# Kernel tuning notes

Hardware: AMD Instinct MI355X
Metric: run time of the kernel (lower is better)

Reference implementation:

```python
import jax, jax.numpy as jnp
import numpy as np

BATCH, SEQ, D_IN, D_OUT = 32, 1024, 128, 128
NEG_SLOPE = 0.1


def setup_inputs() -> dict:
    key = jax.random.key(0)
    k1, k2, k3, k4 = jax.random.split(key, 4)
    nodes = jax.random.normal(k1, (BATCH, SEQ, D_IN), dtype=jnp.float32)
    adjacent = jax.random.randint(k2, (BATCH, SEQ, SEQ), 0, 2, dtype=jnp.int32)
    W = jax.random.normal(k3, (D_IN, D_OUT), dtype=jnp.float32) / np.sqrt(D_IN)
    B = jax.random.normal(k4, (D_IN, D_OUT), dtype=jnp.float32) / np.sqrt(D_IN)
    return {"nodes": nodes, "adjacent": adjacent, "W": W, "B": B}


def reference(nodes, adjacent, W, B):
    # mask[b, out, in] = 1 if edge (out -> in) present
    mask = (adjacent != 0).astype(nodes.dtype)
    # counts[b, in] = in-degree (number of 'out' neighbors pooled per target node)
    counts = mask.sum(axis=1)                               # [b, s_in]
    # segment-sum of neighbor features: pooled[b, in, d] = sum_out mask * nodes[b, out, d]
    pooled = jnp.einsum('boi,bod->bid', mask, nodes)        # [b, s_in, d]
    # mean over neighbors; nodes with zero degree get no pooled contribution
    pooled = jnp.where(counts[..., None] > 0,
                       pooled / jnp.maximum(counts, 1.0)[..., None],
                       jnp.zeros((), dtype=nodes.dtype))
    updated = nodes @ B + pooled @ W                        # [b, s, d_out]
    return jax.nn.leaky_relu(updated, negative_slope=NEG_SLOPE)
```

## Files before the change

### kernel.cpp

```cpp
#include <hip/hip_runtime.h>
#include <hip/hip_bf16.h>

#define SEQ 1024
#define DIM 128
#define NEG_SLOPE 0.1f

typedef __bf16 bf16x8 __attribute__((ext_vector_type(8)));
typedef float f32x4v __attribute__((ext_vector_type(4)));

#define NT_ELEMS (32u * 128u * 1024u)

__device__ __forceinline__ unsigned short bfb(float f) {
    __bf16 h = (__bf16)f;
    return __builtin_bit_cast(unsigned short, h);
}
__device__ __forceinline__ unsigned mpack(int x0, int x1) {
    unsigned m0 = (x0 != 0) ? 0x3F80u : 0u;
    unsigned m1 = (x1 != 0) ? 0x3F80u : 0u;
    return m0 | (m1 << 16);
}

__global__ __launch_bounds__(256)
void transpose_nodes(const float* __restrict__ nodes, unsigned short* __restrict__ nt)
{
    __shared__ float lds[64][33];
    const int bid = blockIdx.x;
    const int b   = bid >> 6;
    const int ot  = (bid >> 2) & 15;
    const int dt  = bid & 3;
    const int o0  = ot * 64, d0 = dt * 32;
    const int tid = threadIdx.x;

    const float* src = nodes + ((size_t)b * SEQ + o0) * DIM + d0;
    #pragma unroll
    for (int p = 0; p < 8; ++p) {
        const int o = (tid >> 5) + p * 8;
        const int d = tid & 31;
        lds[o][d] = src[(size_t)o * DIM + d];
    }
    __syncthreads();
    unsigned short* dst = nt + ((size_t)b * DIM + d0) * SEQ + o0;
    #pragma unroll
    for (int p = 0; p < 4; ++p) {
        const int d  = (tid >> 5) + p * 8;
        const int o2 = (tid & 31) * 2;
        ushort2 v;
        v.x = bfb(lds[o2][d]);
        v.y = bfb(lds[o2 + 1][d]);
        *(ushort2*)(dst + (size_t)d * SEQ + o2) = v;
    }
}

__global__ __launch_bounds__(256)
void transpose_wb(const float* __restrict__ W, const float* __restrict__ Bm,
                  unsigned short* __restrict__ wt, unsigned short* __restrict__ bt)
{
    const int which = blockIdx.x & 1;
    const int slice = blockIdx.x >> 1;
    const float* in  = which ? Bm : W;
    unsigned short* out = which ? bt : wt;
    const int base = slice * 1024;
    #pragma unroll
    for (int r = 0; r < 4; ++r) {
        const int idx = base + r * 256 + threadIdx.x;
        const int d = idx >> 7, k = idx & 127;
        out[idx] = bfb(in[k * DIM + d]);
    }
}

union LdsU {
    unsigned short mask_t[2][64][72];
    unsigned short pooled[64][136];
};

__global__ __launch_bounds__(256, 2)
void gcn_fused(const float* __restrict__ nodes,
               const int* __restrict__ adj,
               const unsigned short* __restrict__ nt,
               const unsigned short* __restrict__ wt,
               const unsigned short* __restrict__ bt,
               float* __restrict__ out)
{
    __shared__ LdsU u;

    const int bid   = blockIdx.x;
    const int xcd   = bid & 7;
    const int slot  = bid >> 3;
    const int batch = ((slot >> 4) << 3) | xcd;
    const int mtile = slot & 15;
    const int i0    = mtile << 6;

    const int tid  = threadIdx.x;
    const int wave = tid >> 6;
    const int lane = tid & 63;
    const int wm   = wave >> 1;
    const int wn   = wave & 1;
    const int lrow = lane & 15;
    const int quad = lane >> 4;

    const int*   __restrict__ adj_b   = adj   + (size_t)batch * SEQ * SEQ;
    const float* __restrict__ nodes_b = nodes + (size_t)batch * SEQ * DIM;
    const unsigned short* __restrict__ nt_b = nt + (size_t)batch * DIM * SEQ;

    const int a_row = (tid >> 4) * 4;
    const int a_col = (tid & 15) * 4;

    f32x4v acc[2][4] = {};
    f32x4v acc_cnt[2] = {};

    bf16x8 ones;
    #pragma unroll
    for (int j = 0; j < 8; ++j) ones[j] = __builtin_bit_cast(__bf16, (unsigned short)0x3F80);

    int4 A[4];
    auto load_adj = [&](int o0) {
        const int* pa = adj_b + (size_t)(o0 + a_row) * SEQ + (i0 + a_col);
        #pragma unroll
        for (int r = 0; r < 4; ++r) A[r] = *(const int4*)(pa + (size_t)r * SEQ);
    };

    const int d_b0 = wn * 64 + lrow;

    load_adj(0);

    for (int n = 0; n < 16; ++n) {
        const int buf = n & 1;
        #pragma unroll
        for (int j = 0; j < 4; ++j) {
            uint2 w;
            w.x = mpack(((const int*)&A[0])[j], ((const int*)&A[1])[j]);
            w.y = mpack(((const int*)&A[2])[j], ((const int*)&A[3])[j]);
            *(uint2*)&u.mask_t[buf][a_col + j][a_row] = w;
        }
        if (n < 15) load_adj((n + 1) * 64);
        __syncthreads();

        const int o_base = n * 64;
        #pragma unroll
        for (int kk = 0; kk < 2; ++kk) {
            const int ko = kk * 32 + quad * 8;
            bf16x8 av[2], bv[4];
            av[0] = *(const bf16x8*)&u.mask_t[buf][wm * 32 + lrow][ko];
            av[1] = *(const bf16x8*)&u.mask_t[buf][wm * 32 + 16 + lrow][ko];
            #pragma unroll
            for (int nf = 0; nf < 4; ++nf)
                bv[nf] = *(const bf16x8*)(nt_b + (size_t)(d_b0 + nf * 16) * SEQ + o_base + ko);
            #pragma unroll
            for (int mf = 0; mf < 2; ++mf) {
                #pragma unroll
                for (int nf = 0; nf < 4; ++nf)
                    acc[mf][nf] = __builtin_amdgcn_mfma_f32_16x16x32_bf16(av[mf], bv[nf], acc[mf][nf], 0, 0, 0);
                acc_cnt[mf] = __builtin_amdgcn_mfma_f32_16x16x32_bf16(av[mf], ones, acc_cnt[mf], 0, 0, 0);
            }
        }
    }

    __syncthreads();
    #pragma unroll
    for (int mf = 0; mf < 2; ++mf) {
        #pragma unroll
        for (int r = 0; r < 4; ++r) {
            const int row = wm * 32 + mf * 16 + quad * 4 + r;
            const float cnt = acc_cnt[mf][r];
            const float inv = (cnt > 0.5f) ? 1.0f / cnt : 0.0f;
            #pragma unroll
            for (int nf = 0; nf < 4; ++nf) {
                const int col = wn * 64 + nf * 16 + lrow;
                u.pooled[row][col] = bfb(acc[mf][nf][r] * inv);
            }
        }
    }
    __syncthreads();

    f32x4v acc2[2][4] = {};

    #pragma unroll
    for (int ks = 0; ks < 4; ++ks) {
        const int k0 = ks * 32 + quad * 8;
        bf16x8 av[2], av2[2], bw[4], bb[4];
        #pragma unroll
        for (int mf = 0; mf < 2; ++mf) {
            av[mf] = *(const bf16x8*)&u.pooled[wm * 32 + mf * 16 + lrow][k0];
            const float* p = nodes_b + (size_t)(i0 + wm * 32 + mf * 16 + lrow) * DIM + k0;
            const float4 f1 = *(const float4*)p;
            const float4 f2 = *(const float4*)(p + 4);
            av2[mf][0] = (__bf16)f1.x; av2[mf][1] = (__bf16)f1.y;
            av2[mf][2] = (__bf16)f1.z; av2[mf][3] = (__bf16)f1.w;
            av2[mf][4] = (__bf16)f2.x; av2[mf][5] = (__bf16)f2.y;
            av2[mf][6] = (__bf16)f2.z; av2[mf][7] = (__bf16)f2.w;
        }
        #pragma unroll
        for (int nf = 0; nf < 4; ++nf) {
            bw[nf] = *(const bf16x8*)(wt + (size_t)(d_b0 + nf * 16) * DIM + k0);
            bb[nf] = *(const bf16x8*)(bt + (size_t)(d_b0 + nf * 16) * DIM + k0);
        }
        #pragma unroll
        for (int mf = 0; mf < 2; ++mf)
            #pragma unroll
            for (int nf = 0; nf < 4; ++nf) {
                acc2[mf][nf] = __builtin_amdgcn_mfma_f32_16x16x32_bf16(av[mf],  bw[nf], acc2[mf][nf], 0, 0, 0);
                acc2[mf][nf] = __builtin_amdgcn_mfma_f32_16x16x32_bf16(av2[mf], bb[nf], acc2[mf][nf], 0, 0, 0);
            }
    }

    float* out_b = out + (size_t)batch * SEQ * DIM;
    #pragma unroll
    for (int mf = 0; mf < 2; ++mf) {
        #pragma unroll
        for (int nf = 0; nf < 4; ++nf) {
            const int col = wn * 64 + nf * 16 + lrow;
            #pragma unroll
            for (int r = 0; r < 4; ++r) {
                const int row = i0 + wm * 32 + mf * 16 + quad * 4 + r;
                const float x = acc2[mf][nf][r];
                out_b[(size_t)row * DIM + col] = (x > 0.0f) ? x : NEG_SLOPE * x;
            }
        }
    }
}

extern "C" void kernel_launch(void* const* d_in, const int* in_sizes, int n_in,
                              void* d_out, int out_size, void* d_ws, size_t ws_size,
                              hipStream_t stream) {
    const float* nodes = (const float*)d_in[0];
    const int*   adj   = (const int*)d_in[1];
    const float* W     = (const float*)d_in[2];
    const float* Bm    = (const float*)d_in[3];
    float*       out   = (float*)d_out;

    unsigned short* nt = (unsigned short*)d_ws;
    unsigned short* wt = nt + NT_ELEMS;
    unsigned short* bt = wt + 16384;

    transpose_nodes<<<dim3(2048), dim3(256), 0, stream>>>(nodes, nt);
    transpose_wb<<<dim3(32), dim3(256), 0, stream>>>(W, Bm, wt, bt);
    gcn_fused<<<dim3(512), dim3(256), 0, stream>>>(nodes, adj, nt, wt, bt, out);
}
```

Baseline: 234.5 us.

## Quantize mask and nodes to FP8, pre-transpose adjacency, use FP8 MFMA

Adds a separate kernel that converts the int32 adjacency into a transposed FP8 (e4m3 one-value) byte mask, and stores transposed nodes as FP8 instead of bf16. The main kernel then reads both directly from global memory, with no LDS staging or barriers in the aggregation loop, and uses fp8 MFMA instructions. The intent is to cut bytes moved and LDS traffic in the hot loop. The cost is an extra full pass over the 128MB adjacency plus a 32MB write, and a much coarser FP8 quantization of node features that may hurt accuracy.

```diff
diff --git a/kernel.cpp b/kernel.cpp
--- a/kernel.cpp
+++ b/kernel.cpp
@@ -7,48 +7,105 @@
 
 typedef __bf16 bf16x8 __attribute__((ext_vector_type(8)));
 typedef float f32x4v __attribute__((ext_vector_type(4)));
-
-#define NT_ELEMS (32u * 128u * 1024u)
+typedef unsigned char uchar;
+
+#define MASKQ_BYTES ((size_t)32 * 1024 * 1024)
+#define NTQ_BYTES   ((size_t)32 * 128 * 1024)
 
 __device__ __forceinline__ unsigned short bfb(float f) {
     __bf16 h = (__bf16)f;
     return __builtin_bit_cast(unsigned short, h);
 }
-__device__ __forceinline__ unsigned mpack(int x0, int x1) {
-    unsigned m0 = (x0 != 0) ? 0x3F80u : 0u;
-    unsigned m1 = (x1 != 0) ? 0x3F80u : 0u;
-    return m0 | (m1 << 16);
+
+
+__device__ __forceinline__ uchar f32_to_e4m3(float f) {
+#if __has_builtin(__builtin_amdgcn_cvt_pk_fp8_f32)
+    int r = __builtin_amdgcn_cvt_pk_fp8_f32(f, f, 0, false);
+    return (uchar)(r & 0xff);
+#else
+    unsigned u = __builtin_bit_cast(unsigned, f);
+    unsigned s = (u >> 24) & 0x80;
+    int e = (u >> 23) & 0xff;
+    unsigned m = u & 0x7fffff;
+    int te = e - 120;
+    if (te >= 1) {
+        unsigned keep = m >> 20, rest = m & 0xfffff;
+        keep += (rest > 0x80000u) || (rest == 0x80000u && (keep & 1));
+        if (keep == 8) { keep = 0; ++te; }
+        if (te > 15) return (uchar)(s | 0x7e);
+        return (uchar)(s | (te << 3) | keep);
+    }
+    float af = f < 0 ? -f : f;
+    int q = (int)(af * 512.0f + 0.5f);
+    if (q > 7) q = 7;
+    return (uchar)(s | q);
+#endif
 }
 
 __global__ __launch_bounds__(256)
-void transpose_nodes(const float* __restrict__ nodes, unsigned short* __restrict__ nt)
+void transpose_adj(const int* __restrict__ adj, uchar* __restrict__ mq)
+{
+    __shared__ uchar lds[64][72];
+    const int b  = blockIdx.x >> 8;
+    const int ot = (blockIdx.x >> 4) & 15;
+    const int it = blockIdx.x & 15;
+    const int o0 = ot << 6, i0 = it << 6;
+    const int t  = threadIdx.x;
+
+    const int r0 = (t >> 4) << 2;
+    const int c0 = (t & 15) << 2;
+    const int* pa = adj + ((size_t)(b * SEQ + o0 + r0)) * SEQ + i0 + c0;
+    int4 A[4];
+    #pragma unroll
+    for (int r = 0; r < 4; ++r) A[r] = *(const int4*)(pa + (size_t)r * SEQ);
+
+    #pragma unroll
+    for (int c = 0; c < 4; ++c) {
+        unsigned w = 0;
+        w |= (((const int*)&A[0])[c] != 0 ? 0x38u : 0u);
+        w |= (((const int*)&A[1])[c] != 0 ? 0x38u : 0u) << 8;
+        w |= (((const int*)&A[2])[c] != 0 ? 0x38u : 0u) << 16;
+        w |= (((const int*)&A[3])[c] != 0 ? 0x38u : 0u) << 24;
+        *(unsigned*)&lds[c0 + c][r0] = w;
+    }
+    __syncthreads();
+
+    const int i_loc = t >> 2;
+    const int quad  = t & 3;
+    const uint2 lo = *(const uint2*)&lds[i_loc][quad * 8];
+    const uint2 hi = *(const uint2*)&lds[i_loc][32 + quad * 8];
+    uint4 outv; outv.x = lo.x; outv.y = lo.y; outv.z = hi.x; outv.w = hi.y;
+    *(uint4*)(mq + ((size_t)(b * SEQ + i0 + i_loc)) * SEQ + o0 + quad * 16) = outv;
+}
+
+__global__ __launch_bounds__(256)
+void transpose_nodes(const float* __restrict__ nodes, uchar* __restrict__ nq)
 {
     __shared__ float lds[64][33];
-    const int bid = blockIdx.x;
-    const int b   = bid >> 6;
-    const int ot  = (bid >> 2) & 15;
-    const int dt  = bid & 3;
-    const int o0  = ot * 64, d0 = dt * 32;
-    const int tid = threadIdx.x;
-
-    const float* src = nodes + ((size_t)b * SEQ + o0) * DIM + d0;
+    const int b  = blockIdx.x >> 6;
+    const int ot = (blockIdx.x >> 2) & 15;
+    const int dt = blockIdx.x & 3;
+    const int o0 = ot << 6, d0 = dt << 5;
+    const int t  = threadIdx.x;
+
+    const float* src = nodes + ((size_t)(b * SEQ + o0)) * DIM + d0;
     #pragma unroll
     for (int p = 0; p < 8; ++p) {
-        const int o = (tid >> 5) + p * 8;
-        const int d = tid & 31;
+        const int o = (t >> 5) + p * 8;
+        const int d = t & 31;
         lds[o][d] = src[(size_t)o * DIM + d];
     }
     __syncthreads();
-    unsigned short* dst = nt + ((size_t)b * DIM + d0) * SEQ + o0;
-    #pragma unroll
-    for (int p = 0; p < 4; ++p) {
-        const int d  = (tid >> 5) + p * 8;
-        const int o2 = (tid & 31) * 2;
-        ushort2 v;
-        v.x = bfb(lds[o2][d]);
-        v.y = bfb(lds[o2 + 1][d]);
-        *(ushort2*)(dst + (size_t)d * SEQ + o2) = v;
-    }
+
+    const int d_loc = t >> 3;
+    const int p0    = (t & 7) * 8;
+    const int quad  = (t & 7) >> 1;
+    const int half  = t & 1;
+    const int ob    = half * 32 + quad * 8;
+    union { uchar b[8]; uint2 u; } pk;
+    #pragma unroll
+    for (int j = 0; j < 8; ++j) pk.b[j] = f32_to_e4m3(lds[ob + j][d_loc]);
+    *(uint2*)(nq + ((size_t)(b * DIM + d0 + d_loc)) * SEQ + o0 + p0) = pk.u;
 }
 
 __global__ __launch_bounds__(256)
@@ -57,7 +114,7 @@
 {
     const int which = blockIdx.x & 1;
     const int slice = blockIdx.x >> 1;
-    const float* in  = which ? Bm : W;
+    const float* in = which ? Bm : W;
     unsigned short* out = which ? bt : wt;
     const int base = slice * 1024;
     #pragma unroll
@@ -68,20 +125,19 @@
     }
 }
 
-union LdsU {
-    unsigned short mask_t[2][64][72];
-    unsigned short pooled[64][136];
-};
+__device__ __forceinline__ long mk64(unsigned lo, unsigned hi) {
+    return (long)(((unsigned long long)hi << 32) | lo);
+}
 
 __global__ __launch_bounds__(256, 2)
-void gcn_fused(const float* __restrict__ nodes,
-               const int* __restrict__ adj,
-               const unsigned short* __restrict__ nt,
-               const unsigned short* __restrict__ wt,
-               const unsigned short* __restrict__ bt,
-               float* __restrict__ out)
-{
-    __shared__ LdsU u;
+void gcn_main(const float* __restrict__ nodes,
+              const uchar* __restrict__ mq,
+              const uchar* __restrict__ nq,
+              const unsigned short* __restrict__ wt,
+              const unsigned short* __restrict__ bt,
+              float* __restrict__ out)
+{
+    __shared__ unsigned short pooled[64][136];
 
     const int bid   = blockIdx.x;
     const int xcd   = bid & 7;
@@ -98,64 +154,48 @@
     const int lrow = lane & 15;
     const int quad = lane >> 4;
 
-    const int*   __restrict__ adj_b   = adj   + (size_t)batch * SEQ * SEQ;
+    const uchar* __restrict__ mq_b = mq + (size_t)batch * SEQ * SEQ;
+    const uchar* __restrict__ nq_b = nq + (size_t)batch * DIM * SEQ;
     const float* __restrict__ nodes_b = nodes + (size_t)batch * SEQ * DIM;
-    const unsigned short* __restrict__ nt_b = nt + (size_t)batch * DIM * SEQ;
-
-    const int a_row = (tid >> 4) * 4;
-    const int a_col = (tid & 15) * 4;
 
     f32x4v acc[2][4] = {};
     f32x4v acc_cnt[2] = {};
-
-    bf16x8 ones;
-    #pragma unroll
-    for (int j = 0; j < 8; ++j) ones[j] = __builtin_bit_cast(__bf16, (unsigned short)0x3F80);
-
-    int4 A[4];
-    auto load_adj = [&](int o0) {
-        const int* pa = adj_b + (size_t)(o0 + a_row) * SEQ + (i0 + a_col);
-        #pragma unroll
-        for (int r = 0; r < 4; ++r) A[r] = *(const int4*)(pa + (size_t)r * SEQ);
-    };
-
-    const int d_b0 = wn * 64 + lrow;
-
-    load_adj(0);
-
+    const long ones = 0x3838383838383838L;
+
+    const uchar* pa0 = mq_b + (size_t)(i0 + wm * 32 + lrow) * SEQ + quad * 16;
+    const uchar* pb0 = nq_b + (size_t)(wn * 64 + lrow) * SEQ + quad * 16;
+
+    #pragma unroll 4
     for (int n = 0; n < 16; ++n) {
-        const int buf = n & 1;
-        #pragma unroll
-        for (int j = 0; j < 4; ++j) {
-            uint2 w;
-            w.x = mpack(((const int*)&A[0])[j], ((const int*)&A[1])[j]);
-            w.y = mpack(((const int*)&A[2])[j], ((const int*)&A[3])[j]);
-            *(uint2*)&u.mask_t[buf][a_col + j][a_row] = w;
-        }
-        if (n < 15) load_adj((n + 1) * 64);
-        __syncthreads();
-
-        const int o_base = n * 64;
-        #pragma unroll
-        for (int kk = 0; kk < 2; ++kk) {
-            const int ko = kk * 32 + quad * 8;
-            bf16x8 av[2], bv[4];
-            av[0] = *(const bf16x8*)&u.mask_t[buf][wm * 32 + lrow][ko];
-            av[1] = *(const bf16x8*)&u.mask_t[buf][wm * 32 + 16 + lrow][ko];
+        const int off = n * 64;
+        uint4 a4[2], b4[4];
+        #pragma unroll
+        for (int mf = 0; mf < 2; ++mf)
+            a4[mf] = *(const uint4*)(pa0 + (size_t)mf * 16 * SEQ + off);
+        #pragma unroll
+        for (int nf = 0; nf < 4; ++nf)
+            b4[nf] = *(const uint4*)(pb0 + (size_t)nf * 16 * SEQ + off);
+        #pragma unroll
+        for (int half = 0; half < 2; ++half) {
+            long a64[2], b64[4];
+            #pragma unroll
+            for (int mf = 0; mf < 2; ++mf)
+                a64[mf] = half ? mk64(a4[mf].z, a4[mf].w) : mk64(a4[mf].x, a4[mf].y);
             #pragma unroll
             for (int nf = 0; nf < 4; ++nf)
-                bv[nf] = *(const bf16x8*)(nt_b + (size_t)(d_b0 + nf * 16) * SEQ + o_base + ko);
+                b64[nf] = half ? mk64(b4[nf].z, b4[nf].w) : mk64(b4[nf].x, b4[nf].y);
             #pragma unroll
             for (int mf = 0; mf < 2; ++mf) {
                 #pragma unroll
                 for (int nf = 0; nf < 4; ++nf)
-                    acc[mf][nf] = __builtin_amdgcn_mfma_f32_16x16x32_bf16(av[mf], bv[nf], acc[mf][nf], 0, 0, 0);
-                acc_cnt[mf] = __builtin_amdgcn_mfma_f32_16x16x32_bf16(av[mf], ones, acc_cnt[mf], 0, 0, 0);
-            }
-        }
-    }
-
-    __syncthreads();
+                    acc[mf][nf] = __builtin_amdgcn_mfma_f32_16x16x32_fp8_fp8(
+                        a64[mf], b64[nf], acc[mf][nf], 0, 0, 0);
+                acc_cnt[mf] = __builtin_amdgcn_mfma_f32_16x16x32_fp8_fp8(
+                    a64[mf], ones, acc_cnt[mf], 0, 0, 0);
+            }
+        }
+    }
+
     #pragma unroll
     for (int mf = 0; mf < 2; ++mf) {
         #pragma unroll
@@ -166,13 +206,14 @@
             #pragma unroll
             for (int nf = 0; nf < 4; ++nf) {
                 const int col = wn * 64 + nf * 16 + lrow;
-                u.pooled[row][col] = bfb(acc[mf][nf][r] * inv);
+                pooled[row][col] = bfb(acc[mf][nf][r] * inv);
             }
         }
     }
     __syncthreads();
 
     f32x4v acc2[2][4] = {};
+    const int d_b0 = wn * 64 + lrow;
 
     #pragma unroll
     for (int ks = 0; ks < 4; ++ks) {
@@ -180,7 +221,7 @@
         bf16x8 av[2], av2[2], bw[4], bb[4];
         #pragma unroll
         for (int mf = 0; mf < 2; ++mf) {
-            av[mf] = *(const bf16x8*)&u.pooled[wm * 32 + mf * 16 + lrow][k0];
+            av[mf] = *(const bf16x8*)&pooled[wm * 32 + mf * 16 + lrow][k0];
             const float* p = nodes_b + (size_t)(i0 + wm * 32 + mf * 16 + lrow) * DIM + k0;
             const float4 f1 = *(const float4*)p;
             const float4 f2 = *(const float4*)(p + 4);
@@ -228,11 +269,13 @@
     const float* Bm    = (const float*)d_in[3];
     float*       out   = (float*)d_out;
 
-    unsigned short* nt = (unsigned short*)d_ws;
-    unsigned short* wt = nt + NT_ELEMS;
+    uchar* mq = (uchar*)d_ws;
+    uchar* nq = mq + MASKQ_BYTES;
+    unsigned short* wt = (unsigned short*)(nq + NTQ_BYTES);
     unsigned short* bt = wt + 16384;
 
-    transpose_nodes<<<dim3(2048), dim3(256), 0, stream>>>(nodes, nt);
-    transpose_wb<<<dim3(32), dim3(256), 0, stream>>>(W, Bm, wt, bt);
-    gcn_fused<<<dim3(512), dim3(256), 0, stream>>>(nodes, adj, nt, wt, bt, out);
-}
+    transpose_adj  <<<dim3(8192), dim3(256), 0, stream>>>(adj, mq);
+    transpose_nodes<<<dim3(2048), dim3(256), 0, stream>>>(nodes, nq);
+    transpose_wb   <<<dim3(32),   dim3(256), 0, stream>>>(W, Bm, wt, bt);
+    gcn_main       <<<dim3(512),  dim3(256), 0, stream>>>(nodes, mq, nq, wt, bt, out);
+}
```

After: 255.2 us. +8.8%, slower.
